# Optimization experiments

Measured on AMD Instinct MI355X. Metric: run time of the kernel, lower is better.

The kernel has to match this reference:

```python
import jax, jax.numpy as jnp
import numpy as np

MU_P = 0.15
MASK_ID = 103
VOCAB = 30522


def setup_inputs() -> dict:
    key = jax.random.key(0)
    k1, k2 = jax.random.split(key)
    B, C, S = 1024, 4, 2048
    # first half = per-token sampling weights, second half = shared_tokens (unused by the math)
    my_attention_mask = jax.random.uniform(k1, (B, C, 2 * S), dtype=jnp.float32)
    attention_mask = jnp.ones((B, C, S), dtype=jnp.int32)  # tokenizer attention mask
    input_ids = jax.random.randint(k2, (B, C, S), 0, VOCAB, dtype=jnp.int32)
    return {"my_attention_mask": my_attention_mask,
            "attention_mask": attention_mask,
            "input_ids": input_ids}


def reference(my_attention_mask, attention_mask, input_ids):
    """Weighted sampling WITHOUT replacement per (batch, choice) row via Gumbel-top-k.

    Original loops over (k, j), draws num_to_mask = floor(sum(tok_mask) * N(mu_p, sigma))
    indices from the nonzero weights in my_attention_mask[..., :S] (prob ~ weight),
    masks those token positions in input_ids and emits the indicator mask.
    Gumbel-top-k: keys = log(w) + Gumbel noise; the top-num_to_mask keys are a
    weighted sample without replacement from w. Zero-weight positions get -inf keys.
    """
    B, C, S = input_ids.shape
    w = my_attention_mask[..., :S]  # [B, C, S] sampling weights

    key = jax.random.key(42)
    kg, kn = jax.random.split(key)
    sigma = min(0.05, MU_P / 4.0)
    frac = MU_P + sigma * jax.random.normal(kn, (B, C), dtype=jnp.float32)
    num_to_mask = jnp.floor(
        attention_mask.sum(axis=-1).astype(jnp.float32) * frac
    ).astype(jnp.int32)  # [B, C]

    log_w = jnp.where(w > 0, jnp.log(jnp.maximum(w, 1e-30)), -jnp.inf)
    keys = log_w + jax.random.gumbel(kg, w.shape, dtype=jnp.float32)  # [B, C, S]

    # rank[i] = position of i in descending key order (double argsort)
    order = jnp.argsort(-keys, axis=-1)
    rank = jnp.argsort(order, axis=-1)
    new_attention_mask = (rank < num_to_mask[..., None]).astype(jnp.int32)  # [B, C, S]

    new_input_ids = jnp.where(new_attention_mask == 1, MASK_ID, input_ids)
    discriminator_labels = -new_attention_mask
    return new_input_ids, new_attention_mask, discriminator_labels
```

## Files before the change

### kernel.cpp

```cpp
#include <hip/hip_runtime.h>
#include <stdint.h>
#include <math.h>

#define SLEN 2048
#define EPT 32
#define NTHREADS 256
#define ROWS_PER_BLOCK 4
#define NCHUNK 8
#define TOKENS_PER_OUT 8388608

__host__ __device__ __forceinline__ void tf2x32(uint32_t k0, uint32_t k1,
                                                uint32_t x0, uint32_t x1,
                                                uint32_t &o0, uint32_t &o1) {
  uint32_t ks2 = 0x1BD11BDAu ^ k0 ^ k1;
  x0 += k0; x1 += k1;
#define TFR(r) { x0 += x1; x1 = (x1 << (r)) | (x1 >> (32 - (r))); x1 ^= x0; }
  TFR(13) TFR(15) TFR(26) TFR(6)
  x0 += k1;  x1 += ks2 + 1u;
  TFR(17) TFR(29) TFR(16) TFR(24)
  x0 += ks2; x1 += k0 + 2u;
  TFR(13) TFR(15) TFR(26) TFR(6)
  x0 += k0;  x1 += k1 + 3u;
  TFR(17) TFR(29) TFR(16) TFR(24)
  x0 += k1;  x1 += ks2 + 4u;
  TFR(13) TFR(15) TFR(26) TFR(6)
  x0 += ks2; x1 += k0 + 5u;
#undef TFR
  o0 = x0; o1 = x1;
}

__device__ __forceinline__ void tf4_bits(uint32_t k0, uint32_t k1,
                                         uint32_t cbase, uint32_t bits[4]) {
  const uint32_t ks2 = 0x1BD11BDAu ^ k0 ^ k1;
  uint32_t x0[4], x1[4];
#pragma unroll
  for (int i = 0; i < 4; ++i) { x0[i] = k0; x1[i] = (cbase + (uint32_t)i) + k1; }
#define TFR4(r)                                                         \
  _Pragma("unroll")                                                     \
  for (int i = 0; i < 4; ++i) {                                         \
    x0[i] += x1[i];                                                     \
    x1[i] = (x1[i] << (r)) | (x1[i] >> (32 - (r)));                     \
    x1[i] ^= x0[i];                                                     \
  }                                                                     \
  __builtin_amdgcn_sched_barrier(0);
#define INJ4(a, b)                                                      \
  _Pragma("unroll")                                                     \
  for (int i = 0; i < 4; ++i) { x0[i] += (a); x1[i] += (b); }
  TFR4(13) TFR4(15) TFR4(26) TFR4(6)
  INJ4(k1, ks2 + 1u)
  TFR4(17) TFR4(29) TFR4(16) TFR4(24)
  INJ4(ks2, k0 + 2u)
  TFR4(13) TFR4(15) TFR4(26) TFR4(6)
  INJ4(k0, k1 + 3u)
  TFR4(17) TFR4(29) TFR4(16) TFR4(24)
  INJ4(k1, ks2 + 4u)
  TFR4(13) TFR4(15) TFR4(26) TFR4(6)
  INJ4(ks2, k0 + 5u)
#undef TFR4
#undef INJ4
#pragma unroll
  for (int i = 0; i < 4; ++i) bits[i] = x0[i] ^ x1[i];
}

__device__ __forceinline__ float u01_from_bits(uint32_t bits) {
  return __uint_as_float((bits >> 9) | 0x3F800000u) - 1.0f;
}

#define SBAR() __builtin_amdgcn_sched_barrier(0)

__device__ __forceinline__ void log8_cr(const float x[8], float out[8]) {
#pragma clang fp contract(off)
  double m[8]; int e[8];
#pragma unroll
  for (int i = 0; i < 8; ++i) {
    uint32_t xb   = __float_as_uint(x[i]);
    uint32_t mant = xb & 0x7FFFFFu;
    int      ee   = (int)(xb >> 23) - 127;
    bool     big  = mant > 0x3504F3u;
    e[i] = ee + (big ? 1 : 0);
    uint32_t hi = (big ? 0x3FE00000u : 0x3FF00000u) | (mant >> 3);
    uint32_t lo = mant << 29;
    m[i] = __longlong_as_double(((long long)hi << 32) | (long long)lo);
  }
  SBAR();
  double mp1[8];
#pragma unroll
  for (int i = 0; i < 8; ++i) mp1[i] = m[i] + 1.0;
  SBAR();
  double y[8];
#pragma unroll
  for (int i = 0; i < 8; ++i) y[i] = __builtin_amdgcn_rcp(mp1[i]);
  SBAR();
#pragma unroll
  for (int i = 0; i < 8; ++i) y[i] = fma(fma(-mp1[i], y[i], 1.0), y[i], y[i]);
  SBAR();
  double r[8];
#pragma unroll
  for (int i = 0; i < 8; ++i) r[i] = (m[i] - 1.0) * y[i];
  SBAR();
  double t[8];
#pragma unroll
  for (int i = 0; i < 8; ++i) t[i] = r[i] * r[i];
  SBAR();
  double p[8];
#pragma unroll
  for (int i = 0; i < 8; ++i) p[i] = fma(0.07692307692307693, t[i], 0.09090909090909091);
  SBAR();
#pragma unroll
  for (int i = 0; i < 8; ++i) p[i] = fma(p[i], t[i], 0.1111111111111111);
  SBAR();
#pragma unroll
  for (int i = 0; i < 8; ++i) p[i] = fma(p[i], t[i], 0.14285714285714285);
  SBAR();
#pragma unroll
  for (int i = 0; i < 8; ++i) p[i] = fma(p[i], t[i], 0.2);
  SBAR();
#pragma unroll
  for (int i = 0; i < 8; ++i) p[i] = fma(p[i], t[i], 0.3333333333333333);
  SBAR();
#pragma unroll
  for (int i = 0; i < 8; ++i) p[i] = fma(p[i], t[i], 1.0);
  SBAR();
#pragma unroll
  for (int i = 0; i < 8; ++i) r[i] = r[i] + r[i];
  SBAR();
#pragma unroll
  for (int i = 0; i < 8; ++i) p[i] = r[i] * p[i];
  SBAR();
#pragma unroll
  for (int i = 0; i < 8; ++i)
    out[i] = (float)fma((double)e[i], 0.6931471805599453, p[i]);
}

__device__ __forceinline__ float log_cr(float x) {
#pragma clang fp contract(off)
  uint32_t xb   = __float_as_uint(x);
  uint32_t mant = xb & 0x7FFFFFu;
  int      e    = (int)(xb >> 23) - 127;
  bool     big  = mant > 0x3504F3u;
  e += big ? 1 : 0;
  uint32_t hi = (big ? 0x3FE00000u : 0x3FF00000u) | (mant >> 3);
  double m = __longlong_as_double(((long long)hi << 32) | (long long)(mant << 29));
  double mp1 = m + 1.0;
  double y = __builtin_amdgcn_rcp(mp1);
  y = fma(fma(-mp1, y, 1.0), y, y);
  double r = (m - 1.0) * y;
  double t = r * r;
  double p = fma(0.07692307692307693, t, 0.09090909090909091);
  p = fma(p, t, 0.1111111111111111);
  p = fma(p, t, 0.14285714285714285);
  p = fma(p, t, 0.2);
  p = fma(p, t, 0.3333333333333333);
  p = fma(p, t, 1.0);
  return (float)fma((double)e, 0.6931471805599453, (r + r) * p);
}

__device__ float erfinv_xla(float x) {
#pragma clang fp contract(off)
  float x2  = x * x;
  float nx2 = -x2;
  float l1p;
  if (fabsf(nx2) < 1e-4f) {
    l1p = (-0.5f * nx2 + 1.0f) * nx2;
  } else {
    l1p = log_cr(1.0f + nx2);
  }
  float w = -l1p;
  float p;
  if (w < 5.0f) {
    float ww = w - 2.5f;
    p = 2.81022636e-08f;
    p = p * ww + 3.43273939e-07f;
    p = p * ww + -3.5233877e-06f;
    p = p * ww + -4.39150654e-06f;
    p = p * ww + 0.00021858087f;
    p = p * ww + -0.00125372503f;
    p = p * ww + -0.00417768164f;
    p = p * ww + 0.246640727f;
    p = p * ww + 1.50140941f;
  } else {
    float ww = sqrtf(w) - 3.0f;
    p = -0.000200214257f;
    p = p * ww + 0.000100950558f;
    p = p * ww + 0.00134934322f;
    p = p * ww + -0.00367342844f;
    p = p * ww + 0.00573950773f;
    p = p * ww + -0.0076224613f;
    p = p * ww + 0.00943887047f;
    p = p * ww + 1.00167406f;
    p = p * ww + 2.83297682f;
  }
  return p * x;
}

__global__ __launch_bounds__(NTHREADS, 4)
void gumbel_topk_mask(const float* __restrict__ wfull,
                      const int*   __restrict__ attn,
                      const int*   __restrict__ ids,
                      int* __restrict__ out,
                      uint32_t kg0, uint32_t kg1, uint32_t kn0, uint32_t kn1) {
#pragma clang fp contract(off)
  const int t    = threadIdx.x;
  const int lane = t & 63;
  const int wid  = t >> 6;
  const int row  = blockIdx.x * ROWS_PER_BLOCK + wid;

  __shared__ __align__(16) uint32_t hist[ROWS_PER_BLOCK][256];

  const size_t rbase = (size_t)row * SLEN;
  const size_t wbase = (size_t)row * (2 * SLEN);

  ((uint4*)hist[wid])[lane] = make_uint4(0u, 0u, 0u, 0u);

  const int4*   av4 = (const int4*)(attn + rbase);
  const float4* wv4 = (const float4*)(wfull + wbase);
  const int4*   iv4 = (const int4*)(ids + rbase);

  int psum = 0;
#pragma unroll
  for (int j = 0; j < NCHUNK; ++j) {
    int4 a = av4[64 * j + lane];
    psum += a.x + a.y + a.z + a.w;
  }
  float4 wv[NCHUNK];
#pragma unroll
  for (int j = 0; j < NCHUNK; ++j) wv[j] = wv4[64 * j + lane];

  uint32_t no0, no1;
  tf2x32(kn0, kn1, 0u, (uint32_t)row, no0, no1);
  float f0  = u01_from_bits(no0 ^ no1);
  float lo  = __uint_as_float(0xBF7FFFFFu);
  float u2  = fmaxf(lo, f0 * 2.0f + lo);
  float z   = erfinv_xla(u2);
  float nrm = 1.4142135623730951f * z;
  float frac = 0.15f + 0.0375f * nrm;

#pragma unroll
  for (int off = 32; off; off >>= 1) psum += __shfl_down(psum, off, 64);
  int asum = __shfl(psum, 0, 64);
  int kk = (int)floorf((float)asum * frac);

  uint32_t mloc[EPT];
#pragma unroll
  for (int c = 0; c < 4; ++c) {
    uint32_t bits[8];
    tf4_bits(kg0, kg1, (uint32_t)(rbase + 256 * (2 * c)     + 4 * lane), bits + 0);
    tf4_bits(kg0, kg1, (uint32_t)(rbase + 256 * (2 * c + 1) + 4 * lane), bits + 4);
    SBAR();
    float4 wa = wv[2 * c], wb = wv[2 * c + 1];
    float wl[8] = {wa.x, wa.y, wa.z, wa.w, wb.x, wb.y, wb.z, wb.w};
    float uu[8];
#pragma unroll
    for (int e = 0; e < 8; ++e) {
      float f = u01_from_bits(bits[e]);
      uu[e] = fmaxf(1.17549435e-38f, f * 1.0f + 1.17549435e-38f);
    }
    SBAR();
    float l1[8];
    log8_cr(uu, l1);
    float wm[8];
#pragma unroll
    for (int e = 0; e < 8; ++e) wm[e] = fmaxf(wl[e], 1e-30f);
    float lw[8];
    log8_cr(wm, lw);
    float nl1[8];
#pragma unroll
    for (int e = 0; e < 8; ++e) nl1[e] = -l1[e];
    float l2[8];
    log8_cr(nl1, l2);
    SBAR();
#pragma unroll
    for (int e = 0; e < 8; ++e) {
      float key = (wl[e] > 0.0f) ? (lw[e] + (-l2[e])) : -__builtin_inff();
      uint32_t kb = __float_as_uint(key);
      mloc[8 * c + e] = (kb & 0x80000000u) ? ~kb : (kb | 0x80000000u);
    }
  }

  int4 idsv[NCHUNK];
#pragma unroll
  for (int j = 0; j < NCHUNK; ++j) idsv[j] = iv4[64 * j + lane];

  uint32_t T, r;
  if (kk <= 0)          { T = 0xFFFFFFFFu; r = 0u; }
  else if (kk >= SLEN)  { T = 0u;          r = (uint32_t)SLEN; }
  else {
    T = 0u;
    uint32_t need = (uint32_t)kk;
    asm volatile("s_waitcnt lgkmcnt(0)" ::: "memory");
#pragma unroll
    for (int e = 0; e < EPT; ++e)
      atomicAdd(&hist[wid][mloc[e] >> 24], 1u);
    for (int p = 3; ; --p) {
      asm volatile("s_waitcnt lgkmcnt(0)" ::: "memory");
      __builtin_amdgcn_wave_barrier();
      uint4 hq = ((const uint4*)hist[wid])[lane];
      uint32_t gs  = hq.x + hq.y + hq.z + hq.w;
      uint32_t sfx = gs;
#pragma unroll
      for (int off = 1; off < 64; off <<= 1) {
        uint32_t n = __shfl_down(sfx, off, 64);
        if (lane + off < 64) sfx += n;
      }
      uint32_t Gex = sfx - gs;
      uint32_t S3 = Gex;
      uint32_t S2 = S3 + hq.w;
      uint32_t S1 = S2 + hq.z;
      uint32_t S0 = S1 + hq.y;
      uint32_t hh[4] = {hq.x, hq.y, hq.z, hq.w};
      uint32_t SS[4] = {S0, S1, S2, S3};
      int haswin = 0; uint32_t binv = 0u, remv = 0u; int donev = 0;
#pragma unroll
      for (int i = 0; i < 4; ++i) {
        if (hh[i] && SS[i] < need && need <= SS[i] + hh[i]) {
          haswin = 1;
          binv = (uint32_t)(4 * lane + i);
          remv = need - SS[i];
          donev = (remv == hh[i]) ? 1 : 0;
        }
      }
      unsigned long long wmask = __ballot(haswin);
      int src = (int)(__ffsll((unsigned long long)wmask) - 1);
      uint32_t bin = (uint32_t)__shfl((int)binv, src, 64);
      uint32_t rem = (uint32_t)__shfl((int)remv, src, 64);
      int     done = __shfl(donev, src, 64);
      T |= bin << (8 * p);
      need = rem;
      if (done || p == 0) { r = rem; break; }
      ((uint4*)hist[wid])[lane] = make_uint4(0u, 0u, 0u, 0u);
      asm volatile("s_waitcnt lgkmcnt(0)" ::: "memory");
      __builtin_amdgcn_wave_barrier();
      const int sh = 8 * p;
#pragma unroll
      for (int e = 0; e < EPT; ++e) {
        uint32_t m = mloc[e];
        if ((m >> sh) == (T >> sh))
          atomicAdd(&hist[wid][(m >> (sh - 8)) & 255u], 1u);
      }
    }
  }

  uint32_t cnt[NCHUNK];
#pragma unroll
  for (int j = 0; j < NCHUNK; ++j) {
    uint32_t c = 0;
#pragma unroll
    for (int e = 0; e < 4; ++e) c += (mloc[4 * j + e] == T) ? 1u : 0u;
    cnt[j] = c;
  }
  uint32_t incl[4];
#pragma unroll
  for (int q = 0; q < 4; ++q) incl[q] = cnt[2 * q] | (cnt[2 * q + 1] << 16);
#pragma unroll
  for (int off = 1; off < 64; off <<= 1) {
#pragma unroll
    for (int q = 0; q < 4; ++q) {
      uint32_t n = __shfl_up(incl[q], off, 64);
      if (lane >= off) incl[q] += n;
    }
  }
  uint32_t Spre[NCHUNK], tot[NCHUNK];
#pragma unroll
  for (int q = 0; q < 4; ++q) {
    uint32_t t63 = (uint32_t)__shfl((int)incl[q], 63, 64);
    tot[2 * q]      = t63 & 0xFFFFu;
    tot[2 * q + 1]  = t63 >> 16;
    Spre[2 * q]     = (incl[q] & 0xFFFFu) - cnt[2 * q];
    Spre[2 * q + 1] = (incl[q] >> 16)     - cnt[2 * q + 1];
  }

  int4* po = (int4*)(out + rbase);
  int4* pm = (int4*)(out + TOKENS_PER_OUT + rbase);
  int4* pl = (int4*)(out + 2 * TOKENS_PER_OUT + rbase);
  uint32_t C = 0;
#pragma unroll
  for (int j = 0; j < NCHUNK; ++j) {
    uint32_t excl = C + Spre[j];
    int4 iv = idsv[j];
    int idv[4] = {iv.x, iv.y, iv.z, iv.w};
    int oid[4], omk[4], olb[4];
#pragma unroll
    for (int e = 0; e < 4; ++e) {
      uint32_t m = mloc[4 * j + e];
      bool eq  = (m == T);
      bool msk = (m > T) || (eq && (excl < r));
      excl += eq ? 1u : 0u;
      oid[e] = msk ? 103 : idv[e];
      omk[e] = msk ? 1 : 0;
      olb[e] = msk ? -1 : 0;
    }
    po[64 * j + lane] = make_int4(oid[0], oid[1], oid[2], oid[3]);
    pm[64 * j + lane] = make_int4(omk[0], omk[1], omk[2], omk[3]);
    pl[64 * j + lane] = make_int4(olb[0], olb[1], olb[2], olb[3]);
    C += tot[j];
  }
}

extern "C" void kernel_launch(void* const* d_in, const int* in_sizes, int n_in,
                              void* d_out, int out_size, void* d_ws, size_t ws_size,
                              hipStream_t stream) {
  (void)n_in; (void)d_ws; (void)ws_size; (void)out_size;
  const float* wfull = (const float*)d_in[0];
  const int*   attn  = (const int*)d_in[1];
  const int*   ids   = (const int*)d_in[2];
  int* out = (int*)d_out;

  uint32_t kg0, kg1, kn0, kn1, o0, o1;
  tf2x32(0u, 42u, 0u, 0u, o0, o1); kg0 = o0; kg1 = o1;
  tf2x32(0u, 42u, 0u, 1u, o0, o1); kn0 = o0; kn1 = o1;

  int rows = in_sizes[1] / SLEN;
  hipLaunchKernelGGL(gumbel_topk_mask, dim3(rows / ROWS_PER_BLOCK), dim3(NTHREADS),
                     0, stream, wfull, attn, ids, out, kg0, kg1, kn0, kn1);
}
```

Before: 208.5 us.

## Split each row across two waves with shared histogram radix select

Each row of 2048 tokens is now handled by a 128-thread block of two wavefronts, each owning half the row with 16 elements per thread, instead of one wavefront per row. The radix-select histogram becomes shared and double-buffered across the two waves, and the block synchronises for the attention sum, each histogram pass and the tie-count prefix. This halves per-thread register state and the serial work per row, raising occupancy and parallelism. The cost is block-level barriers and shared-memory atomic contention between the two waves on every pass.

```diff
diff --git a/kernel.cpp b/kernel.cpp
--- a/kernel.cpp
+++ b/kernel.cpp
@@ -3,10 +3,9 @@
 #include <math.h>
 
 #define SLEN 2048
-#define EPT 32
-#define NTHREADS 256
-#define ROWS_PER_BLOCK 4
-#define NCHUNK 8
+#define EPT 16
+#define NTHREADS 128
+#define CPW 4
 #define TOKENS_PER_OUT 8388608
 
 __host__ __device__ __forceinline__ void tf2x32(uint32_t k0, uint32_t k1,
@@ -193,7 +192,7 @@
   return p * x;
 }
 
-__global__ __launch_bounds__(NTHREADS, 4)
+__global__ __launch_bounds__(NTHREADS, 8)
 void gumbel_topk_mask(const float* __restrict__ wfull,
                       const int*   __restrict__ attn,
                       const int*   __restrict__ ids,
@@ -203,14 +202,16 @@
   const int t    = threadIdx.x;
   const int lane = t & 63;
   const int wid  = t >> 6;
-  const int row  = blockIdx.x * ROWS_PER_BLOCK + wid;
-
-  __shared__ __align__(16) uint32_t hist[ROWS_PER_BLOCK][256];
+  const int row  = blockIdx.x;
+
+  __shared__ __align__(16) uint32_t hist[2][256];
+  __shared__ uint32_t wsum[2];
+  __shared__ uint32_t wtot[2];
 
   const size_t rbase = (size_t)row * SLEN;
   const size_t wbase = (size_t)row * (2 * SLEN);
 
-  ((uint4*)hist[wid])[lane] = make_uint4(0u, 0u, 0u, 0u);
+  ((uint2*)hist[0])[64 * wid + lane] = make_uint2(0u, 0u);
 
   const int4*   av4 = (const int4*)(attn + rbase);
   const float4* wv4 = (const float4*)(wfull + wbase);
@@ -218,13 +219,10 @@
 
   int psum = 0;
 #pragma unroll
-  for (int j = 0; j < NCHUNK; ++j) {
-    int4 a = av4[64 * j + lane];
+  for (int j = 0; j < CPW; ++j) {
+    int4 a = av4[64 * (CPW * wid + j) + lane];
     psum += a.x + a.y + a.z + a.w;
   }
-  float4 wv[NCHUNK];
-#pragma unroll
-  for (int j = 0; j < NCHUNK; ++j) wv[j] = wv4[64 * j + lane];
 
   uint32_t no0, no1;
   tf2x32(kn0, kn1, 0u, (uint32_t)row, no0, no1);
@@ -237,17 +235,18 @@
 
 #pragma unroll
   for (int off = 32; off; off >>= 1) psum += __shfl_down(psum, off, 64);
-  int asum = __shfl(psum, 0, 64);
-  int kk = (int)floorf((float)asum * frac);
+  if (lane == 0) wsum[wid] = (uint32_t)psum;
 
   uint32_t mloc[EPT];
 #pragma unroll
-  for (int c = 0; c < 4; ++c) {
+  for (int c = 0; c < 2; ++c) {
+    const int g0 = CPW * wid + 2 * c;
+    float4 wa = wv4[64 * g0 + lane];
+    float4 wb = wv4[64 * (g0 + 1) + lane];
     uint32_t bits[8];
-    tf4_bits(kg0, kg1, (uint32_t)(rbase + 256 * (2 * c)     + 4 * lane), bits + 0);
-    tf4_bits(kg0, kg1, (uint32_t)(rbase + 256 * (2 * c + 1) + 4 * lane), bits + 4);
+    tf4_bits(kg0, kg1, (uint32_t)(rbase + 256 * g0 + 4 * lane), bits + 0);
+    tf4_bits(kg0, kg1, (uint32_t)(rbase + 256 * (g0 + 1) + 4 * lane), bits + 4);
     SBAR();
-    float4 wa = wv[2 * c], wb = wv[2 * c + 1];
     float wl[8] = {wa.x, wa.y, wa.z, wa.w, wb.x, wb.y, wb.z, wb.w};
     float uu[8];
 #pragma unroll
@@ -277,9 +276,13 @@
     }
   }
 
-  int4 idsv[NCHUNK];
-#pragma unroll
-  for (int j = 0; j < NCHUNK; ++j) idsv[j] = iv4[64 * j + lane];
+  int4 idsv[CPW];
+#pragma unroll
+  for (int j = 0; j < CPW; ++j) idsv[j] = iv4[64 * (CPW * wid + j) + lane];
+
+  __syncthreads();
+  int asum = (int)(wsum[0] + wsum[1]);
+  int kk = (int)floorf((float)asum * frac);
 
   uint32_t T, r;
   if (kk <= 0)          { T = 0xFFFFFFFFu; r = 0u; }
@@ -287,14 +290,14 @@
   else {
     T = 0u;
     uint32_t need = (uint32_t)kk;
-    asm volatile("s_waitcnt lgkmcnt(0)" ::: "memory");
 #pragma unroll
     for (int e = 0; e < EPT; ++e)
-      atomicAdd(&hist[wid][mloc[e] >> 24], 1u);
+      atomicAdd(&hist[0][mloc[e] >> 24], 1u);
+    int cur = 0;
     for (int p = 3; ; --p) {
-      asm volatile("s_waitcnt lgkmcnt(0)" ::: "memory");
-      __builtin_amdgcn_wave_barrier();
-      uint4 hq = ((const uint4*)hist[wid])[lane];
+      __syncthreads();
+      uint4 hq = ((const uint4*)hist[cur])[lane];
+      ((uint2*)hist[cur ^ 1])[64 * wid + lane] = make_uint2(0u, 0u);
       uint32_t gs  = hq.x + hq.y + hq.z + hq.w;
       uint32_t sfx = gs;
 #pragma unroll
@@ -327,54 +330,55 @@
       T |= bin << (8 * p);
       need = rem;
       if (done || p == 0) { r = rem; break; }
-      ((uint4*)hist[wid])[lane] = make_uint4(0u, 0u, 0u, 0u);
-      asm volatile("s_waitcnt lgkmcnt(0)" ::: "memory");
-      __builtin_amdgcn_wave_barrier();
+      __syncthreads();
       const int sh = 8 * p;
 #pragma unroll
       for (int e = 0; e < EPT; ++e) {
         uint32_t m = mloc[e];
         if ((m >> sh) == (T >> sh))
-          atomicAdd(&hist[wid][(m >> (sh - 8)) & 255u], 1u);
+          atomicAdd(&hist[cur ^ 1][(m >> (sh - 8)) & 255u], 1u);
       }
+      cur ^= 1;
     }
   }
 
-  uint32_t cnt[NCHUNK];
-#pragma unroll
-  for (int j = 0; j < NCHUNK; ++j) {
+  uint32_t cnt[CPW];
+#pragma unroll
+  for (int j = 0; j < CPW; ++j) {
     uint32_t c = 0;
 #pragma unroll
     for (int e = 0; e < 4; ++e) c += (mloc[4 * j + e] == T) ? 1u : 0u;
     cnt[j] = c;
   }
-  uint32_t incl[4];
-#pragma unroll
-  for (int q = 0; q < 4; ++q) incl[q] = cnt[2 * q] | (cnt[2 * q + 1] << 16);
+  uint32_t incl[2];
+#pragma unroll
+  for (int q = 0; q < 2; ++q) incl[q] = cnt[2 * q] | (cnt[2 * q + 1] << 16);
 #pragma unroll
   for (int off = 1; off < 64; off <<= 1) {
 #pragma unroll
-    for (int q = 0; q < 4; ++q) {
+    for (int q = 0; q < 2; ++q) {
       uint32_t n = __shfl_up(incl[q], off, 64);
       if (lane >= off) incl[q] += n;
     }
   }
-  uint32_t Spre[NCHUNK], tot[NCHUNK];
-#pragma unroll
-  for (int q = 0; q < 4; ++q) {
+  uint32_t Spre[CPW], tot[CPW];
+#pragma unroll
+  for (int q = 0; q < 2; ++q) {
     uint32_t t63 = (uint32_t)__shfl((int)incl[q], 63, 64);
     tot[2 * q]      = t63 & 0xFFFFu;
     tot[2 * q + 1]  = t63 >> 16;
     Spre[2 * q]     = (incl[q] & 0xFFFFu) - cnt[2 * q];
     Spre[2 * q + 1] = (incl[q] >> 16)     - cnt[2 * q + 1];
   }
+  if (lane == 0) wtot[wid] = tot[0] + tot[1] + tot[2] + tot[3];
+  __syncthreads();
+  uint32_t C = wid ? wtot[0] : 0u;
 
   int4* po = (int4*)(out + rbase);
   int4* pm = (int4*)(out + TOKENS_PER_OUT + rbase);
   int4* pl = (int4*)(out + 2 * TOKENS_PER_OUT + rbase);
-  uint32_t C = 0;
-#pragma unroll
-  for (int j = 0; j < NCHUNK; ++j) {
+#pragma unroll
+  for (int j = 0; j < CPW; ++j) {
     uint32_t excl = C + Spre[j];
     int4 iv = idsv[j];
     int idv[4] = {iv.x, iv.y, iv.z, iv.w};
@@ -389,9 +393,10 @@
       omk[e] = msk ? 1 : 0;
       olb[e] = msk ? -1 : 0;
     }
-    po[64 * j + lane] = make_int4(oid[0], oid[1], oid[2], oid[3]);
-    pm[64 * j + lane] = make_int4(omk[0], omk[1], omk[2], omk[3]);
-    pl[64 * j + lane] = make_int4(olb[0], olb[1], olb[2], olb[3]);
+    const int gi = 64 * (CPW * wid + j) + lane;
+    po[gi] = make_int4(oid[0], oid[1], oid[2], oid[3]);
+    pm[gi] = make_int4(omk[0], omk[1], omk[2], omk[3]);
+    pl[gi] = make_int4(olb[0], olb[1], olb[2], olb[3]);
     C += tot[j];
   }
 }
@@ -410,6 +415,6 @@
   tf2x32(0u, 42u, 0u, 1u, o0, o1); kn0 = o0; kn1 = o1;
 
   int rows = in_sizes[1] / SLEN;
-  hipLaunchKernelGGL(gumbel_topk_mask, dim3(rows / ROWS_PER_BLOCK), dim3(NTHREADS),
+  hipLaunchKernelGGL(gumbel_topk_mask, dim3(rows), dim3(NTHREADS),
                      0, stream, wfull, attn, ids, out, kg0, kg1, kn0, kn1);
 }
```

Measured after the change: 213.1 us. 1.02x slower.
